# Kernel tuning notes

Measured on AMD Instinct MI355X. Metric: run time of the kernel, lower is better.

## Reference

```python
import jax, jax.numpy as jnp
import numpy as np

N = 200000   # nodes
E = 400000   # edges
G = 4096     # graphs in batch
F_IN = 77    # atom feature dim
D = 128      # dim_drug
L = 3        # layer_drug
BN_EPS = 1e-5


def setup_inputs() -> dict:
    key = jax.random.key(0)
    ks = jax.random.split(key, 16)
    inp = {}
    inp["x"] = jax.random.normal(ks[0], (N, F_IN), jnp.float32)
    inp["edge_index"] = jax.random.randint(ks[1], (2, E), 0, N, dtype=jnp.int64)
    inp["batch"] = jnp.sort(jax.random.randint(ks[2], (N,), 0, G, dtype=jnp.int64))
    dims = [F_IN, D, D]
    i = 3
    for l in range(L):
        din = dims[l]
        inp[f"w1_{l}"] = jax.random.normal(ks[i], (din, D), jnp.float32) / np.sqrt(din); i += 1
        inp[f"b1_{l}"] = jnp.zeros((D,), jnp.float32)
        inp[f"w2_{l}"] = jax.random.normal(ks[i], (D, D), jnp.float32) / np.sqrt(D); i += 1
        inp[f"b2_{l}"] = jnp.zeros((D,), jnp.float32)
        inp[f"gamma_{l}"] = jnp.ones((D,), jnp.float32)
        inp[f"beta_{l}"] = jnp.zeros((D,), jnp.float32)
    inp["w_emb"] = jax.random.normal(ks[i], (L * D, 256), jnp.float32) / np.sqrt(L * D)
    inp["b_emb"] = jnp.zeros((256,), jnp.float32)
    return inp


def _gin_bn_layer(h, src, dst, w1, b1, w2, b2, gamma, beta):
    # GINConv (eps=0): out_i = MLP(x_i + sum_{j->i} x_j)
    agg = jax.ops.segment_sum(h[src], dst, num_segments=N)  # scatter-add aggregation
    h = h + agg
    h = jax.nn.relu(h @ w1 + b1) @ w2 + b2                  # GIN MLP
    h = jax.nn.relu(h)                                       # outer F.relu
    mu = jnp.mean(h, axis=0)
    var = jnp.var(h, axis=0)                                  # biased var (training-mode BN)
    return (h - mu) * jax.lax.rsqrt(var + BN_EPS) * gamma + beta


def reference(x, edge_index, batch,
              w1_0, b1_0, w2_0, b2_0, gamma_0, beta_0,
              w1_1, b1_1, w2_1, b2_1, gamma_1, beta_1,
              w1_2, b1_2, w2_2, b2_2, gamma_2, beta_2,
              w_emb, b_emb):
    src, dst = edge_index[0], edge_index[1]
    layers = [(w1_0, b1_0, w2_0, b2_0, gamma_0, beta_0),
              (w1_1, b1_1, w2_1, b2_1, gamma_1, beta_1),
              (w1_2, b1_2, w2_2, b2_2, gamma_2, beta_2)]
    h = x
    outs = []
    for (w1, b1, w2, b2, g, b) in layers:
        h = _gin_bn_layer(h, src, dst, w1, b1, w2, b2, g, b)
        outs.append(h)
    node_rep = jnp.concatenate(outs, axis=1)                  # JK 'cat' -> [N, L*D]
    pooled = jax.ops.segment_max(node_rep, batch, num_segments=G)  # global_max_pool -> [G, L*D]
    # drug_emb: Linear -> ReLU -> Dropout (identity in eval)
    return jax.nn.relu(pooled @ w_emb + b_emb)
```

## Files before the change

kernel.cpp:

```cpp
#include <hip/hip_runtime.h>
#include <hip/hip_bf16.h>
#include <float.h>

#define NN 200000
#define NE 400000
#define NG 4096
#define FIN 77
#define DD 128
#define BN_EPS 1e-5f
#define NB_SCAN ((NN + 255) / 256)
#define NBLK (NN / 64)
#define WCAP 1024

#define GS_BLKS 17
#define CNT_BLKS ((NE + 255) / 256)
#define XCONV_BLKS (NN * 12 / 256)
#define WCONV_BLKS 192

typedef float f32x4 __attribute__((ext_vector_type(4)));
typedef short s16x8 __attribute__((ext_vector_type(8)));

__device__ __forceinline__ unsigned short f2bf(float x) {
    unsigned b = __float_as_uint(x);
    unsigned r = (b + 0x7FFFu + ((b >> 16) & 1u)) >> 16;
    return (unsigned short)r;
}
__device__ __forceinline__ float bf2f(unsigned short u) {
    return __uint_as_float(((unsigned)u) << 16);
}

__device__ __forceinline__ int load_idx(const void* p, int is64, long long i) {
    return is64 ? (int)((const long long*)p)[i] : ((const int*)p)[i];
}

__device__ __forceinline__ void derive_ss(const float* __restrict__ sums,
                                          const float* __restrict__ gamma,
                                          const float* __restrict__ beta,
                                          int c, float& sc, float& sh) {
    float mu = sums[c] * (1.f / (float)NN);
    float var = sums[DD + c] * (1.f / (float)NN) - mu * mu;
    sc = gamma[c] * rsqrtf(var + BN_EPS);
    sh = beta[c] - mu * sc;
}

__global__ __launch_bounds__(256) void prep_kernel(
    const float* __restrict__ x, unsigned short* __restrict__ xb,
    const float* __restrict__ w10, const float* __restrict__ w20,
    const float* __restrict__ w11, const float* __restrict__ w21,
    const float* __restrict__ w12, const float* __restrict__ w22,
    unsigned short* __restrict__ wtb,
    const void* __restrict__ eidx, const void* __restrict__ batch,
    int* __restrict__ start, int* __restrict__ deg, int* __restrict__ flags)
{
    int b = blockIdx.x;
    if (b < GS_BLKS) {
        __shared__ int sb64;
        if (threadIdx.x == 0) {
            int b64 = 1;
            const unsigned* bw = (const unsigned*)batch;
            for (int i = 0; i < 16; i++) if (bw[NN - 1 - 2 * i] != 0u) b64 = 0;
            sb64 = b64;
        }
        __syncthreads();
        int is64 = sb64;
        int g = b * 256 + threadIdx.x;
        if (g > NG) return;
        int lo = 0, hi = NN;
        while (lo < hi) {
            int mid = (lo + hi) >> 1;
            int v = load_idx(batch, is64, mid);
            if (v < g) lo = mid + 1; else hi = mid;
        }
        start[g] = lo;
    } else if (b < GS_BLKS + CNT_BLKS) {
        __shared__ int se64;
        if (threadIdx.x == 0) {
            int e64 = 1;
            const unsigned* ew = (const unsigned*)eidx;
            for (int i = 0; i < 16; i++) if (ew[2 * NE - 1 - 2 * i] != 0u) e64 = 0;
            se64 = e64;
        }
        __syncthreads();
        int e = (b - GS_BLKS) * 256 + threadIdx.x;
        if (e >= NE) return;
        int dst = load_idx(eidx, se64, (long long)NE + e);
        atomicAdd(&deg[dst], 1);
    } else if (b < GS_BLKS + CNT_BLKS + XCONV_BLKS) {
        int idx = (b - GS_BLKS - CNT_BLKS) * 256 + threadIdx.x;
        int row = idx / 12, c8 = (idx % 12) * 8;
        union { s16x8 v; unsigned short u[8]; } pk;
#pragma unroll
        for (int j = 0; j < 8; j++) {
            int c = c8 + j;
            pk.u[j] = (c < FIN) ? f2bf(x[(long long)row * FIN + c]) : (unsigned short)0;
        }
        *(s16x8*)&xb[(long long)row * 96 + c8] = pk.v;
    } else if (b < GS_BLKS + CNT_BLKS + XCONV_BLKS + WCONV_BLKS) {
        int bb = b - GS_BLKS - CNT_BLKS - XCONV_BLKS;
        int l = bb >> 6;
        int idx = (bb & 63) * 256 + threadIdx.x;
        int c = idx >> 7, k = idx & 127;
        const float* w1 = (l == 0) ? w10 : ((l == 1) ? w11 : w12);
        const float* w2 = (l == 0) ? w20 : ((l == 1) ? w21 : w22);
        int K1 = (l == 0) ? FIN : DD;
        unsigned short* wt1 = wtb + l * 2 * 16384;
        wt1[idx] = f2bf(k < K1 ? w1[k * DD + c] : 0.f);
        wt1[16384 + idx] = f2bf(w2[k * DD + c]);
    } else {
        if (threadIdx.x == 0) {
            int e64 = 1, b64 = 1;
            const unsigned* ew = (const unsigned*)eidx;
            const unsigned* bw = (const unsigned*)batch;
            for (int i = 0; i < 16; i++) {
                if (ew[2 * NE - 1 - 2 * i] != 0u) e64 = 0;
                if (bw[NN - 1 - 2 * i] != 0u) b64 = 0;
            }
            flags[0] = e64;
            flags[1] = b64;
        }
    }
}

__global__ void scan1_kernel(const int* __restrict__ deg, int* __restrict__ incl,
                             int* __restrict__ bsum) {
    __shared__ int sh[256];
    int i = blockIdx.x * 256 + threadIdx.x;
    int v = (i < NN) ? deg[i] : 0;
    sh[threadIdx.x] = v;
    __syncthreads();
    for (int off = 1; off < 256; off <<= 1) {
        int t = (threadIdx.x >= off) ? sh[threadIdx.x - off] : 0;
        __syncthreads();
        sh[threadIdx.x] += t;
        __syncthreads();
    }
    if (i < NN) incl[i] = sh[threadIdx.x];
    if (threadIdx.x == 255) bsum[blockIdx.x] = sh[255];
}

__global__ __launch_bounds__(256) void scan23_kernel(
    const int* __restrict__ incl, const int* __restrict__ deg,
    const int* __restrict__ bsum, int* __restrict__ rowptr, int* __restrict__ cursor) {
    __shared__ int red[256];
    int b = blockIdx.x;
    int t = threadIdx.x;
    int s = 0;
    for (int i = t; i < b; i += 256) s += bsum[i];
    red[t] = s;
    __syncthreads();
    for (int off = 128; off > 0; off >>= 1) {
        if (t < off) red[t] += red[t + off];
        __syncthreads();
    }
    int pfx = red[0];
    int i = b * 256 + t;
    if (i < NN) {
        int ex = pfx + incl[i] - deg[i];
        rowptr[i] = ex;
        cursor[i] = ex;
    }
    if (i == 0) rowptr[NN] = NE;
}

__global__ void fill_kernel(const void* __restrict__ eidx, const int* __restrict__ flags,
                            int* __restrict__ cursor, int* __restrict__ slots) {
    int e = blockIdx.x * 256 + threadIdx.x;
    if (e >= NE) return;
    int is64 = flags[0];
    int src = load_idx(eidx, is64, e);
    int dst = load_idx(eidx, is64, (long long)NE + e);
    int pos = atomicAdd(&cursor[dst], 1);
    slots[pos] = src;
}

template <int L0>
__global__ __launch_bounds__(512, 8) void fused_layer(
    const unsigned short* __restrict__ src,
    const float* __restrict__ sums_prev, const float* __restrict__ gm_prev,
    const float* __restrict__ bt_prev,
    const int* __restrict__ rowptr, const int* __restrict__ slots,
    const unsigned short* __restrict__ wt1, const unsigned short* __restrict__ wt2,
    const float* __restrict__ b1, const float* __restrict__ b2,
    unsigned short* __restrict__ out, float* __restrict__ sums_out)
{
    __shared__ unsigned short Xs[64 * 128];
    __shared__ int s_lo[65];
    __shared__ int s_win[WCAP];
    constexpr int SK = L0 ? 96 : 128;
    constexpr int KS1 = L0 ? 3 : 4;
    int tid = threadIdx.x;
    int lane = tid & 63;
    int w = tid >> 6;
    int rowBase = blockIdx.x * 64;

    int wb = rowptr[rowBase];
    int wn = rowptr[rowBase + 64] - wb;
    if (tid < 65) s_lo[tid] = rowptr[rowBase + tid];
    int wcap = (wn < WCAP) ? wn : WCAP;
    for (int i = tid; i < wcap; i += 512) s_win[i] = slots[wb + i];
    __syncthreads();

    {
        int rp = tid >> 4;
        int c8 = (tid & 15) * 8;
        float sc[8], sh[8];
        if (!L0) {
#pragma unroll
            for (int j = 0; j < 8; j++)
                derive_ss(sums_prev, gm_prev, bt_prev, c8 + j, sc[j], sh[j]);
        }
        int rA = rp, rB = 32 + rp;
        int griA = rowBase + rA, griB = rowBase + rB;
        bool skip = (L0 && c8 >= 96);
        s16x8 voA = {}, v0A = {}, v1A = {}, voB = {}, v0B = {}, v1B = {};
        int dA = 0, dB = 0, loA = 0, loB = 0, oA = 0, oB = 0;
        float mA0 = 0.f, mA1 = 0.f, mB0 = 0.f, mB1 = 0.f;
        if (!skip) {
            loA = s_lo[rA]; dA = s_lo[rA + 1] - loA; oA = loA - wb;
            loB = s_lo[rB]; dB = s_lo[rB + 1] - loB; oB = loB - wb;
            int iA0 = (dA > 0) ? ((oA < WCAP) ? s_win[oA] : slots[loA]) : griA;
            int iA1 = (dA > 1) ? ((oA + 1 < WCAP) ? s_win[oA + 1] : slots[loA + 1]) : griA;
            int iB0 = (dB > 0) ? ((oB < WCAP) ? s_win[oB] : slots[loB]) : griB;
            int iB1 = (dB > 1) ? ((oB + 1 < WCAP) ? s_win[oB + 1] : slots[loB + 1]) : griB;
            voA = *(const s16x8*)&src[griA * SK + c8];
            v0A = *(const s16x8*)&src[iA0 * SK + c8];
            v1A = *(const s16x8*)&src[iA1 * SK + c8];
            voB = *(const s16x8*)&src[griB * SK + c8];
            v0B = *(const s16x8*)&src[iB0 * SK + c8];
            v1B = *(const s16x8*)&src[iB1 * SK + c8];
            mA0 = (dA > 0) ? 1.f : 0.f; mA1 = (dA > 1) ? 1.f : 0.f;
            mB0 = (dB > 0) ? 1.f : 0.f; mB1 = (dB > 1) ? 1.f : 0.f;
        }
        float aA[8], aB[8];
#pragma unroll
        for (int j = 0; j < 8; j++) {
            aA[j] = bf2f((unsigned short)voA[j]) + mA0 * bf2f((unsigned short)v0A[j])
                                                 + mA1 * bf2f((unsigned short)v1A[j]);
            aB[j] = bf2f((unsigned short)voB[j]) + mB0 * bf2f((unsigned short)v0B[j])
                                                 + mB1 * bf2f((unsigned short)v1B[j]);
        }
        if (!skip) {
            for (int k = 2; k < dA; k++) {
                int kk = oA + k;
                int sid = (kk < WCAP) ? s_win[kk] : slots[loA + k];
                s16x8 vk = *(const s16x8*)&src[sid * SK + c8];
#pragma unroll
                for (int j = 0; j < 8; j++) aA[j] += bf2f((unsigned short)vk[j]);
            }
            for (int k = 2; k < dB; k++) {
                int kk = oB + k;
                int sid = (kk < WCAP) ? s_win[kk] : slots[loB + k];
                s16x8 vk = *(const s16x8*)&src[sid * SK + c8];
#pragma unroll
                for (int j = 0; j < 8; j++) aB[j] += bf2f((unsigned short)vk[j]);
            }
            if (!L0) {
                float cntA = (float)(dA + 1), cntB = (float)(dB + 1);
#pragma unroll
                for (int j = 0; j < 8; j++) {
                    aA[j] = aA[j] * sc[j] + cntA * sh[j];
                    aB[j] = aB[j] * sc[j] + cntB * sh[j];
                }
            }
        } else {
#pragma unroll
            for (int j = 0; j < 8; j++) { aA[j] = 0.f; aB[j] = 0.f; }
        }
        union { s16x8 v; unsigned short u[8]; } pkA, pkB;
#pragma unroll
        for (int j = 0; j < 8; j++) { pkA.u[j] = f2bf(aA[j]); pkB.u[j] = f2bf(aB[j]); }
        *(s16x8*)&Xs[rA * 128 + (c8 ^ ((rA & 7) << 3))] = pkA.v;
        *(s16x8*)&Xs[rB * 128 + (c8 ^ ((rB & 7) << 3))] = pkB.v;
    }

    int colbase = w * 16 + (lane & 15);
    s16x8 w1f[4];
    float bs1;
#pragma unroll
    for (int ks = 0; ks < KS1; ks++)
        w1f[ks] = *(const s16x8*)&wt1[colbase * 128 + ks * 32 + (lane >> 4) * 8];
    bs1 = b1[colbase];

    __syncthreads();

    f32x4 acc[4];
#pragma unroll
    for (int rb = 0; rb < 4; rb++) acc[rb] = 0;
#pragma unroll
    for (int ks = 0; ks < KS1; ks++) {
        int lk = ks * 32 + (lane >> 4) * 8;
        s16x8 af[4];
#pragma unroll
        for (int rb = 0; rb < 4; rb++) {
            int r = rb * 16 + (lane & 15);
            af[rb] = *(const s16x8*)&Xs[r * 128 + (lk ^ ((r & 7) << 3))];
        }
#pragma unroll
        for (int rb = 0; rb < 4; rb++)
            acc[rb] = __builtin_amdgcn_mfma_f32_16x16x32_bf16(af[rb], w1f[ks], acc[rb], 0, 0, 0);
    }

    __syncthreads();

#pragma unroll
    for (int rb = 0; rb < 4; rb++) {
#pragma unroll
        for (int reg = 0; reg < 4; reg++) {
            int row = rb * 16 + (lane >> 4) * 4 + reg;
            float v = fmaxf(acc[rb][reg] + bs1, 0.f);
            Xs[row * 128 + (colbase ^ ((row & 7) << 3))] = f2bf(v);
        }
    }

    s16x8 w2f[4];
    float bs2;
#pragma unroll
    for (int ks = 0; ks < 4; ks++)
        w2f[ks] = *(const s16x8*)&wt2[colbase * 128 + ks * 32 + (lane >> 4) * 8];
    bs2 = b2[colbase];

    __syncthreads();

#pragma unroll
    for (int rb = 0; rb < 4; rb++) acc[rb] = 0;
#pragma unroll
    for (int ks = 0; ks < 4; ks++) {
        int lk = ks * 32 + (lane >> 4) * 8;
        s16x8 af[4];
#pragma unroll
        for (int rb = 0; rb < 4; rb++) {
            int r = rb * 16 + (lane & 15);
            af[rb] = *(const s16x8*)&Xs[r * 128 + (lk ^ ((r & 7) << 3))];
        }
#pragma unroll
        for (int rb = 0; rb < 4; rb++)
            acc[rb] = __builtin_amdgcn_mfma_f32_16x16x32_bf16(af[rb], w2f[ks], acc[rb], 0, 0, 0);
    }

    float ps = 0.f, pq = 0.f;
#pragma unroll
    for (int rb = 0; rb < 4; rb++) {
#pragma unroll
        for (int reg = 0; reg < 4; reg++) {
            int row = rowBase + rb * 16 + (lane >> 4) * 4 + reg;
            float v = fmaxf(acc[rb][reg] + bs2, 0.f);
            unsigned short ub = f2bf(v);
            out[row * DD + colbase] = ub;
            float vb = bf2f(ub);
            ps += vb;
            pq += vb * vb;
        }
    }
    ps += __shfl_xor(ps, 16); ps += __shfl_xor(ps, 32);
    pq += __shfl_xor(pq, 16); pq += __shfl_xor(pq, 32);
    if (lane < 16) {
        atomicAdd(&sums_out[colbase], ps);
        atomicAdd(&sums_out[DD + colbase], pq);
    }
}

__global__ __launch_bounds__(256) void pool_kernel(const unsigned short* __restrict__ hm,
                                                   const float* __restrict__ sums,
                                                   const float* __restrict__ gamma,
                                                   const float* __restrict__ beta,
                                                   const int* __restrict__ start,
                                                   float* __restrict__ pooled, int l) {
    __shared__ float red[16][128];
    int g = blockIdx.x;
    int rp = threadIdx.x >> 4;
    int c8 = (threadIdx.x & 15) * 8;
    int lo = start[g], hi = start[g + 1];
    float sc[8], sh[8];
#pragma unroll
    for (int j = 0; j < 8; j++) derive_ss(sums, gamma, beta, c8 + j, sc[j], sh[j]);
    float m[8];
#pragma unroll
    for (int j = 0; j < 8; j++) m[j] = -FLT_MAX;
    for (int n = lo + rp; n < hi; n += 16) {
        s16x8 v = *(const s16x8*)&hm[(long long)n * DD + c8];
#pragma unroll
        for (int j = 0; j < 8; j++)
            m[j] = fmaxf(m[j], bf2f((unsigned short)v[j]) * sc[j] + sh[j]);
    }
#pragma unroll
    for (int j = 0; j < 8; j++) red[rp][c8 + j] = m[j];
    __syncthreads();
    if (threadIdx.x < 128) {
        int c = threadIdx.x;
        float mm = red[0][c];
#pragma unroll
        for (int r = 1; r < 16; r++) mm = fmaxf(mm, red[r][c]);
        pooled[(long long)g * (3 * DD) + l * DD + c] = mm;
    }
}

__global__ __launch_bounds__(256) void emb_kernel(const float* __restrict__ pooled,
                                                  const float* __restrict__ w,
                                                  const float* __restrict__ b,
                                                  float* __restrict__ out) {
    __shared__ float pl[8][384];
    int tid = threadIdx.x;
    int g0 = blockIdx.x * 8;
#pragma unroll
    for (int i = 0; i < 12; i++) {
        int idx = tid + i * 256;
        int gg = idx / 384, c = idx % 384;
        pl[gg][c] = pooled[(long long)(g0 + gg) * 384 + c];
    }
    __syncthreads();
    float acc[8];
#pragma unroll
    for (int gg = 0; gg < 8; gg++) acc[gg] = 0.f;
    for (int k = 0; k < 384; k++) {
        float wv = w[k * 256 + tid];
#pragma unroll
        for (int gg = 0; gg < 8; gg++) acc[gg] += pl[gg][k] * wv;
    }
    float bb = b[tid];
#pragma unroll
    for (int gg = 0; gg < 8; gg++)
        out[(long long)(g0 + gg) * 256 + tid] = fmaxf(acc[gg] + bb, 0.f);
}

extern "C" void kernel_launch(void* const* d_in, const int* in_sizes, int n_in,
                              void* d_out, int out_size, void* d_ws, size_t ws_size,
                              hipStream_t stream) {
    const float* x = (const float*)d_in[0];
    const void* eidx = d_in[1];
    const void* batch = d_in[2];
    const float* w1[3] = { (const float*)d_in[3],  (const float*)d_in[9],  (const float*)d_in[15] };
    const float* b1[3] = { (const float*)d_in[4],  (const float*)d_in[10], (const float*)d_in[16] };
    const float* w2[3] = { (const float*)d_in[5],  (const float*)d_in[11], (const float*)d_in[17] };
    const float* b2[3] = { (const float*)d_in[6],  (const float*)d_in[12], (const float*)d_in[18] };
    const float* gm[3] = { (const float*)d_in[7],  (const float*)d_in[13], (const float*)d_in[19] };
    const float* bt[3] = { (const float*)d_in[8],  (const float*)d_in[14], (const float*)d_in[20] };
    const float* w_emb = (const float*)d_in[21];
    const float* b_emb = (const float*)d_in[22];
    float* out = (float*)d_out;

    unsigned short* R1 = (unsigned short*)d_ws;
    unsigned short* R2 = R1 + (size_t)NN * DD;
    float* pooled = (float*)(R2 + (size_t)NN * DD);
    unsigned short* wtb = (unsigned short*)(pooled + (size_t)NG * 384);
    float* sums = (float*)(wtb + 6 * 16384);
    int* pad = (int*)(sums + 3 * 256);
    int* deg = pad + 8;
    size_t zbytes = (3 * 256) * sizeof(float) + 8 * sizeof(int) + (size_t)NN * sizeof(int);
    int* incl = deg + NN;
    int* bsum = incl + NN;
    int* rowptr = bsum + NB_SCAN;
    int* cursor = rowptr + NN + 1;
    int* slots = cursor + NN;
    int* start = slots + NE;
    int* flags = start + NG + 1;

    hipMemsetAsync(sums, 0, zbytes, stream);

    prep_kernel<<<GS_BLKS + CNT_BLKS + XCONV_BLKS + WCONV_BLKS + 1, 256, 0, stream>>>(
        x, R1, w1[0], w2[0], w1[1], w2[1], w1[2], w2[2], wtb,
        eidx, batch, start, deg, flags);

    scan1_kernel<<<NB_SCAN, 256, 0, stream>>>(deg, incl, bsum);
    scan23_kernel<<<NB_SCAN, 256, 0, stream>>>(incl, deg, bsum, rowptr, cursor);
    fill_kernel<<<(NE + 255) / 256, 256, 0, stream>>>(eidx, flags, cursor, slots);

    unsigned short* hin[3] = { R1, R2, R1 };
    unsigned short* hout[3] = { R2, R1, R2 };
    for (int l = 0; l < 3; l++) {
        const unsigned short* wt1 = wtb + l * 2 * 16384;
        const unsigned short* wt2 = wt1 + 16384;
        float* sums_l = sums + l * 256;
        if (l == 0)
            fused_layer<1><<<NBLK, 512, 0, stream>>>(hin[l], nullptr, nullptr, nullptr,
                                                     rowptr, slots, wt1, wt2,
                                                     b1[l], b2[l], hout[l], sums_l);
        else
            fused_layer<0><<<NBLK, 512, 0, stream>>>(hin[l], sums + (l - 1) * 256,
                                                     gm[l - 1], bt[l - 1],
                                                     rowptr, slots, wt1, wt2,
                                                     b1[l], b2[l], hout[l], sums_l);
        pool_kernel<<<NG, 256, 0, stream>>>(hout[l], sums_l, gm[l], bt[l], start, pooled, l);
    }
    emb_kernel<<<NG / 8, 256, 0, stream>>>(pooled, w_emb, b_emb, out);
}
```

Baseline: 431.2 us.

## Replace BN stat atomics with per-block partials and a finalize kernel

Each fused layer block now writes its column sum and sum-of-squares partials to a buffer instead of issuing atomics on a shared 256-entry array. A new reduction kernel sums the partials, and the last block to finish computes per-channel BN scale and shift once. Downstream layer and pool kernels read these precomputed values instead of re-deriving them. This removes atomic contention and redundant rsqrt work, at the cost of an extra kernel launch and a partials buffer round trip per layer.

```diff
diff --git a/kernel.cpp b/kernel.cpp
--- a/kernel.cpp
+++ b/kernel.cpp
@@ -31,16 +31,6 @@
 
 __device__ __forceinline__ int load_idx(const void* p, int is64, long long i) {
     return is64 ? (int)((const long long*)p)[i] : ((const int*)p)[i];
-}
-
-__device__ __forceinline__ void derive_ss(const float* __restrict__ sums,
-                                          const float* __restrict__ gamma,
-                                          const float* __restrict__ beta,
-                                          int c, float& sc, float& sh) {
-    float mu = sums[c] * (1.f / (float)NN);
-    float var = sums[DD + c] * (1.f / (float)NN) - mu * mu;
-    sc = gamma[c] * rsqrtf(var + BN_EPS);
-    sh = beta[c] - mu * sc;
 }
 
 __global__ __launch_bounds__(256) void prep_kernel(
@@ -175,13 +165,11 @@
 
 template <int L0>
 __global__ __launch_bounds__(512, 8) void fused_layer(
-    const unsigned short* __restrict__ src,
-    const float* __restrict__ sums_prev, const float* __restrict__ gm_prev,
-    const float* __restrict__ bt_prev,
+    const unsigned short* __restrict__ src, const float* __restrict__ ss,
     const int* __restrict__ rowptr, const int* __restrict__ slots,
     const unsigned short* __restrict__ wt1, const unsigned short* __restrict__ wt2,
     const float* __restrict__ b1, const float* __restrict__ b2,
-    unsigned short* __restrict__ out, float* __restrict__ sums_out)
+    unsigned short* __restrict__ out, float* __restrict__ partials)
 {
     __shared__ unsigned short Xs[64 * 128];
     __shared__ int s_lo[65];
@@ -206,8 +194,7 @@
         float sc[8], sh[8];
         if (!L0) {
 #pragma unroll
-            for (int j = 0; j < 8; j++)
-                derive_ss(sums_prev, gm_prev, bt_prev, c8 + j, sc[j], sh[j]);
+            for (int j = 0; j < 8; j++) { sc[j] = ss[c8 + j]; sh[j] = ss[DD + c8 + j]; }
         }
         int rA = rp, rB = 32 + rp;
         int griA = rowBase + rA, griB = rowBase + rB;
@@ -354,15 +341,37 @@
     ps += __shfl_xor(ps, 16); ps += __shfl_xor(ps, 32);
     pq += __shfl_xor(pq, 16); pq += __shfl_xor(pq, 32);
     if (lane < 16) {
-        atomicAdd(&sums_out[colbase], ps);
-        atomicAdd(&sums_out[DD + colbase], pq);
+        partials[(long long)blockIdx.x * 256 + colbase] = ps;
+        partials[(long long)blockIdx.x * 256 + 128 + colbase] = pq;
+    }
+}
+
+__global__ __launch_bounds__(256) void bn_red2_fin_kernel(
+    const float* __restrict__ partials, float* __restrict__ sums, int* __restrict__ done,
+    const float* __restrict__ gamma, const float* __restrict__ beta, float* __restrict__ ss) {
+    float s = 0.f;
+    for (int b = blockIdx.x; b < NBLK; b += gridDim.x)
+        s += partials[(long long)b * 256 + threadIdx.x];
+    atomicAdd(&sums[threadIdx.x], s);
+    __threadfence();
+    __syncthreads();
+    __shared__ int tick;
+    if (threadIdx.x == 0) tick = atomicAdd(done, 1);
+    __syncthreads();
+    if (tick == (int)gridDim.x - 1 && threadIdx.x < 128) {
+        int c = threadIdx.x;
+        float s0 = atomicAdd(&sums[c], 0.f);
+        float s1 = atomicAdd(&sums[DD + c], 0.f);
+        float mu = s0 / (float)NN;
+        float var = s1 / (float)NN - mu * mu;
+        float sc = gamma[c] * rsqrtf(var + BN_EPS);
+        ss[c] = sc;
+        ss[DD + c] = beta[c] - mu * sc;
     }
 }
 
 __global__ __launch_bounds__(256) void pool_kernel(const unsigned short* __restrict__ hm,
-                                                   const float* __restrict__ sums,
-                                                   const float* __restrict__ gamma,
-                                                   const float* __restrict__ beta,
+                                                   const float* __restrict__ ss,
                                                    const int* __restrict__ start,
                                                    float* __restrict__ pooled, int l) {
     __shared__ float red[16][128];
@@ -372,7 +381,7 @@
     int lo = start[g], hi = start[g + 1];
     float sc[8], sh[8];
 #pragma unroll
-    for (int j = 0; j < 8; j++) derive_ss(sums, gamma, beta, c8 + j, sc[j], sh[j]);
+    for (int j = 0; j < 8; j++) { sc[j] = ss[c8 + j]; sh[j] = ss[DD + c8 + j]; }
     float m[8];
 #pragma unroll
     for (int j = 0; j < 8; j++) m[j] = -FLT_MAX;
@@ -441,10 +450,12 @@
     unsigned short* R1 = (unsigned short*)d_ws;
     unsigned short* R2 = R1 + (size_t)NN * DD;
     float* pooled = (float*)(R2 + (size_t)NN * DD);
-    unsigned short* wtb = (unsigned short*)(pooled + (size_t)NG * 384);
-    float* sums = (float*)(wtb + 6 * 16384);
-    int* pad = (int*)(sums + 3 * 256);
-    int* deg = pad + 8;
+    float* partials = pooled + (size_t)NG * 384;
+    unsigned short* wtb = (unsigned short*)(partials + (size_t)NBLK * 256);
+    float* ss = (float*)(wtb + 6 * 16384);
+    float* sums = ss + 3 * 256;
+    int* done = (int*)(sums + 3 * 256);
+    int* deg = done + 8;
     size_t zbytes = (3 * 256) * sizeof(float) + 8 * sizeof(int) + (size_t)NN * sizeof(int);
     int* incl = deg + NN;
     int* bsum = incl + NN;
@@ -469,17 +480,16 @@
     for (int l = 0; l < 3; l++) {
         const unsigned short* wt1 = wtb + l * 2 * 16384;
         const unsigned short* wt2 = wt1 + 16384;
-        float* sums_l = sums + l * 256;
+        float* ss_l = ss + l * 256;
         if (l == 0)
-            fused_layer<1><<<NBLK, 512, 0, stream>>>(hin[l], nullptr, nullptr, nullptr,
-                                                     rowptr, slots, wt1, wt2,
-                                                     b1[l], b2[l], hout[l], sums_l);
+            fused_layer<1><<<NBLK, 512, 0, stream>>>(hin[l], nullptr, rowptr, slots, wt1, wt2,
+                                                     b1[l], b2[l], hout[l], partials);
         else
-            fused_layer<0><<<NBLK, 512, 0, stream>>>(hin[l], sums + (l - 1) * 256,
-                                                     gm[l - 1], bt[l - 1],
-                                                     rowptr, slots, wt1, wt2,
-                                                     b1[l], b2[l], hout[l], sums_l);
-        pool_kernel<<<NG, 256, 0, stream>>>(hout[l], sums_l, gm[l], bt[l], start, pooled, l);
+            fused_layer<0><<<NBLK, 512, 0, stream>>>(hin[l], ss + (l - 1) * 256, rowptr, slots,
+                                                     wt1, wt2, b1[l], b2[l], hout[l], partials);
+        bn_red2_fin_kernel<<<256, 256, 0, stream>>>(partials, sums + l * 256, done + l,
+                                                    gm[l], bt[l], ss_l);
+        pool_kernel<<<NG, 256, 0, stream>>>(hout[l], ss_l, start, pooled, l);
     }
     emb_kernel<<<NG / 8, 256, 0, stream>>>(pooled, w_emb, b_emb, out);
 }
```

Measured after the change: 353.4 us, median of 2. 1.22x faster.
